# Performance work log

Measured on AMD Instinct MI355X. Metric: run time of the kernel, lower is better.

## Reference

```python
import jax, jax.numpy as jnp
import numpy as np

N_QUBITS = 4
N_LAYERS = 1
B, D_IN, D_OUT = 65536, 1024, 1024

def _cnot_perm(c, t):
    idx = np.arange(16)
    cb = (idx >> (3 - c)) & 1
    return idx ^ (cb << (3 - t))  # involutive permutation

CNOT_PERMS = [_cnot_perm(i, (i + 1) % N_QUBITS) for i in range(N_QUBITS)]
_idx = np.arange(16)
Z_SIGNS = np.stack([1.0 - 2.0 * ((_idx >> (3 - i)) & 1) for i in range(N_QUBITS)]).astype(np.float32)  # [4,16]
H_GATE = (np.array([[1, 1], [1, -1]]) / np.sqrt(2.0)).astype(np.complex64)

def _apply_1q(psi, U, wire):
    # psi: [B,2,2,2,2]; U: [2,2] (shared across batch)
    psi = jnp.moveaxis(psi, wire + 1, -1)
    psi = jnp.einsum('b...j,ij->b...i', psi, U)
    return jnp.moveaxis(psi, -1, wire + 1)

def _apply_1q_batched(psi, U, wire):
    # U: [B,2,2] (per-sample gate)
    psi = jnp.moveaxis(psi, wire + 1, -1)
    psi = jnp.einsum('b...j,bij->b...i', psi, U)
    return jnp.moveaxis(psi, -1, wire + 1)

def _ry_batched(th):
    c = jnp.cos(th / 2).astype(jnp.complex64)
    s = jnp.sin(th / 2).astype(jnp.complex64)
    return jnp.stack([jnp.stack([c, -s], -1), jnp.stack([s, c], -1)], -2)  # [B,2,2]

def _rz_batched(th):
    e = jnp.exp(-0.5j * th)  # complex64
    z = jnp.zeros_like(e)
    return jnp.stack([jnp.stack([e, z], -1), jnp.stack([z, jnp.conj(e)], -1)], -2)

def _rot(phi, th, om):
    # PennyLane Rot(phi,theta,omega) = RZ(omega) RY(theta) RZ(phi)
    c = jnp.cos(th / 2)
    s = jnp.sin(th / 2)
    return jnp.stack([
        jnp.stack([jnp.exp(-0.5j * (phi + om)) * c, -jnp.exp(0.5j * (phi - om)) * s]),
        jnp.stack([jnp.exp(-0.5j * (phi - om)) * s, jnp.exp(0.5j * (phi + om)) * c])])

def _circuit(angles, weights):
    # angles: [B,4] float; weights: [n_layers,4,3]; returns <Z_i> per wire: [B,4]
    b = angles.shape[0]
    psi = jnp.zeros((b, 16), jnp.complex64).at[:, 0].set(1.0).reshape(b, 2, 2, 2, 2)
    H = jnp.asarray(H_GATE)
    for i in range(N_QUBITS):
        psi = _apply_1q(psi, H, i)
        f = angles[:, i]
        psi = _apply_1q_batched(psi, _ry_batched(jnp.arctan(f)), i)
        psi = _apply_1q_batched(psi, _rz_batched(jnp.arctan(f ** 2)), i)
    for l in range(N_LAYERS):
        for i in range(N_QUBITS):
            psi = psi.reshape(b, 16)[:, CNOT_PERMS[i]].reshape(b, 2, 2, 2, 2)
        for i in range(N_QUBITS):
            U = _rot(weights[l, i, 0], weights[l, i, 1], weights[l, i, 2])
            psi = _apply_1q(psi, U, i)
    psi_f = psi.reshape(b, 16)
    probs = psi_f.real ** 2 + psi_f.imag ** 2  # [B,16] float32
    return probs @ jnp.asarray(Z_SIGNS).T  # [B,4]

def setup_inputs() -> dict:
    key = jax.random.key(0)
    k = jax.random.split(key, 6)
    scale_pre = 1.0 / np.sqrt(D_IN)
    scale_post = 1.0 / np.sqrt(N_QUBITS)
    return {
        'x': jax.random.normal(k[0], (B, D_IN), jnp.float32),
        'pre_w': jax.random.normal(k[1], (N_QUBITS, D_IN), jnp.float32) * scale_pre,
        'pre_b': jax.random.normal(k[2], (N_QUBITS,), jnp.float32) * scale_pre,
        'q_weights': jax.random.uniform(k[3], (N_LAYERS, N_QUBITS, 3), jnp.float32) * (2.0 * np.pi),
        'post_w': jax.random.normal(k[4], (D_OUT, N_QUBITS), jnp.float32) * scale_post,
        'post_b': jax.random.normal(k[5], (D_OUT,), jnp.float32) * scale_post,
    }

def reference(x, pre_w, pre_b, q_weights, post_w, post_b):
    h = jnp.tanh(x @ pre_w.T + pre_b) * np.pi  # [B,4]
    z = _circuit(h, q_weights).astype(jnp.float32)  # [B,4]
    return z @ post_w.T + post_b  # [B,1024]
```

## Files before the change

kernel.cpp:

```cpp
#include <hip/hip_runtime.h>
#include <math.h>

#define D_IN_K  1024
#define D_OUT_K 1024

static constexpr float PI_F = 3.14159265358979323846f;

__device__ __forceinline__ float dot4(float4 a, float4 b, float acc) {
    return fmaf(a.x, b.x, fmaf(a.y, b.y, fmaf(a.z, b.z, fmaf(a.w, b.w, acc))));
}

template <int MASK>
__device__ __forceinline__ void apply1q(
    float* pr, float* pim,
    float u00r, float u00i, float u01r, float u01i,
    float u10r, float u10i, float u11r, float u11i)
{
#pragma unroll
    for (int j = 0; j < 16; ++j) {
        if (j & MASK) continue;
        const int k = j | MASK;
        float a0r = pr[j], a0i = pim[j], a1r = pr[k], a1i = pim[k];
        pr[j]  = u00r * a0r - u00i * a0i + u01r * a1r - u01i * a1i;
        pim[j] = u00r * a0i + u00i * a0r + u01r * a1i + u01i * a1r;
        pr[k]  = u10r * a0r - u10i * a0i + u11r * a1r - u11i * a1i;
        pim[k] = u10r * a0i + u10i * a0r + u11r * a1i + u11i * a1r;
    }
}

template <int CMASK, int TMASK>
__device__ __forceinline__ void cnot(float* pr, float* pim)
{
#pragma unroll
    for (int j = 0; j < 16; ++j) {
        if ((j & CMASK) && !(j & TMASK)) {
            const int k = j | TMASK;
            float t;
            t = pr[j];  pr[j]  = pr[k];  pr[k]  = t;
            t = pim[j]; pim[j] = pim[k]; pim[k] = t;
        }
    }
}

template <int MASK>
__device__ __forceinline__ void encode_qubit(float* pr, float* pim, float f)
{
    const float r = 0.70710678118654752440f;
    apply1q<MASK>(pr, pim, r, 0.f, r, 0.f, r, 0.f, -r, 0.f);
    float th = atanf(f) * 0.5f;
    float s, c;
    sincosf(th, &s, &c);
    apply1q<MASK>(pr, pim, c, 0.f, -s, 0.f, s, 0.f, c, 0.f);
    float al = atanf(f * f) * 0.5f;
    float sa, ca;
    sincosf(al, &sa, &ca);
    apply1q<MASK>(pr, pim, ca, -sa, 0.f, 0.f, 0.f, 0.f, ca, sa);
}

template <int MASK>
__device__ __forceinline__ void rot_qubit(float* pr, float* pim,
                                          float phi, float th, float om)
{
    float st, ct, sp, cp, sm, cm;
    sincosf(0.5f * th, &st, &ct);
    sincosf(0.5f * (phi + om), &sp, &cp);
    sincosf(0.5f * (phi - om), &sm, &cm);
    apply1q<MASK>(pr, pim,
                  ct * cp, -ct * sp,
                  -st * cm, -st * sm,
                  st * cm, -st * sm,
                  ct * cp, ct * sp);
}

__global__ __launch_bounds__(256) void fused_kernel(
    const float* __restrict__ x, const float* __restrict__ pw,
    const float* __restrict__ pb, const float* __restrict__ qw,
    const float* __restrict__ postw, const float* __restrict__ postb,
    float* __restrict__ out, int B)
{
    const int t    = threadIdx.x;
    const int wave = t >> 6;
    const int lane = t & 63;
    const int row0  = blockIdx.x * 16;
    const int wrow0 = row0 + wave * 4;
    if (row0 >= B) return;

    __shared__ float4 zlds[16];

    const float4* pwv4 = reinterpret_cast<const float4*>(postw);
    float4 w[4];
    float bias[4];
#pragma unroll
    for (int j = 0; j < 4; ++j) {
        w[j]    = pwv4[t + 256 * j];
        bias[j] = postb[t + 256 * j];
    }

    const float4* w0 = reinterpret_cast<const float4*>(pw);
    const float4* w1 = reinterpret_cast<const float4*>(pw + D_IN_K);
    const float4* w2 = reinterpret_cast<const float4*>(pw + 2 * D_IN_K);
    const float4* w3 = reinterpret_cast<const float4*>(pw + 3 * D_IN_K);
    const float4* x0 = reinterpret_cast<const float4*>(x + (size_t)(wrow0 + 0) * D_IN_K);
    const float4* x1 = reinterpret_cast<const float4*>(x + (size_t)(wrow0 + 1) * D_IN_K);
    const float4* x2 = reinterpret_cast<const float4*>(x + (size_t)(wrow0 + 2) * D_IN_K);
    const float4* x3 = reinterpret_cast<const float4*>(x + (size_t)(wrow0 + 3) * D_IN_K);

    float acc[4][4];
#pragma unroll
    for (int r = 0; r < 4; ++r)
#pragma unroll
        for (int q = 0; q < 4; ++q) acc[r][q] = 0.f;

#pragma unroll
    for (int k = 0; k < 4; ++k) {
        const int idx = lane + (k << 6);
        float4 a = w0[idx], b = w1[idx], c = w2[idx], d = w3[idx];
        float4 xv;
        xv = x0[idx];
        acc[0][0] = dot4(xv, a, acc[0][0]); acc[0][1] = dot4(xv, b, acc[0][1]);
        acc[0][2] = dot4(xv, c, acc[0][2]); acc[0][3] = dot4(xv, d, acc[0][3]);
        xv = x1[idx];
        acc[1][0] = dot4(xv, a, acc[1][0]); acc[1][1] = dot4(xv, b, acc[1][1]);
        acc[1][2] = dot4(xv, c, acc[1][2]); acc[1][3] = dot4(xv, d, acc[1][3]);
        xv = x2[idx];
        acc[2][0] = dot4(xv, a, acc[2][0]); acc[2][1] = dot4(xv, b, acc[2][1]);
        acc[2][2] = dot4(xv, c, acc[2][2]); acc[2][3] = dot4(xv, d, acc[2][3]);
        xv = x3[idx];
        acc[3][0] = dot4(xv, a, acc[3][0]); acc[3][1] = dot4(xv, b, acc[3][1]);
        acc[3][2] = dot4(xv, c, acc[3][2]); acc[3][3] = dot4(xv, d, acc[3][3]);
    }

#pragma unroll
    for (int off = 1; off < 64; off <<= 1) {
#pragma unroll
        for (int r = 0; r < 4; ++r)
#pragma unroll
            for (int q = 0; q < 4; ++q)
                acc[r][q] += __shfl_xor(acc[r][q], off, 64);
    }

    if (lane < 4) {
        const int r = lane;
        float hq[4];
#pragma unroll
        for (int q = 0; q < 4; ++q)
            hq[q] = tanhf(acc[r][q] + pb[q]) * PI_F;

        float pr[16], pim[16];
#pragma unroll
        for (int j = 0; j < 16; ++j) { pr[j] = 0.f; pim[j] = 0.f; }
        pr[0] = 1.f;

        encode_qubit<8>(pr, pim, hq[0]);
        encode_qubit<4>(pr, pim, hq[1]);
        encode_qubit<2>(pr, pim, hq[2]);
        encode_qubit<1>(pr, pim, hq[3]);

        cnot<8, 4>(pr, pim);
        cnot<4, 2>(pr, pim);
        cnot<2, 1>(pr, pim);
        cnot<1, 8>(pr, pim);

        rot_qubit<8>(pr, pim, qw[0], qw[1], qw[2]);
        rot_qubit<4>(pr, pim, qw[3], qw[4], qw[5]);
        rot_qubit<2>(pr, pim, qw[6], qw[7], qw[8]);
        rot_qubit<1>(pr, pim, qw[9], qw[10], qw[11]);

        float z0 = 0.f, z1 = 0.f, z2 = 0.f, z3 = 0.f;
#pragma unroll
        for (int j = 0; j < 16; ++j) {
            float p = pr[j] * pr[j] + pim[j] * pim[j];
            z0 += (j & 8) ? -p : p;
            z1 += (j & 4) ? -p : p;
            z2 += (j & 2) ? -p : p;
            z3 += (j & 1) ? -p : p;
        }
        float4 zv; zv.x = z0; zv.y = z1; zv.z = z2; zv.w = z3;
        zlds[wave * 4 + r] = zv;
    }
    __syncthreads();

#pragma unroll
    for (int r = 0; r < 16; ++r) {
        float4 zr = zlds[r];
        float* orow = out + (size_t)(row0 + r) * D_OUT_K;
#pragma unroll
        for (int j = 0; j < 4; ++j) {
            float o = fmaf(zr.x, w[j].x,
                      fmaf(zr.y, w[j].y,
                      fmaf(zr.z, w[j].z,
                      fmaf(zr.w, w[j].w, bias[j]))));
            orow[t + 256 * j] = o;
        }
    }
}

extern "C" void kernel_launch(void* const* d_in, const int* in_sizes, int n_in,
                              void* d_out, int out_size, void* d_ws, size_t ws_size,
                              hipStream_t stream)
{
    const float* x      = (const float*)d_in[0];
    const float* pre_w  = (const float*)d_in[1];
    const float* pre_b  = (const float*)d_in[2];
    const float* qw     = (const float*)d_in[3];
    const float* post_w = (const float*)d_in[4];
    const float* post_b = (const float*)d_in[5];
    float* out = (float*)d_out;

    const int B = in_sizes[0] / D_IN_K;

    (void)d_ws; (void)ws_size;

    fused_kernel<<<(B + 15) / 16, 256, 0, stream>>>(
        x, pre_w, pre_b, qw, post_w, post_b, out, B);
}
```

Baseline: 445.5 us.

## Distribute quantum statevector across lanes and replace trig with algebraic identities

The 16-amplitude statevector simulation is now spread so each lane holds one amplitude, with one 16-lane group per batch row. It no longer runs serially in 4 lanes while 60 idle. The encoding stage is computed as a product state using cos/sin of half-arctan derived via sqrt identities instead of atanf/sincosf. CNOTs become lane shuffles, and the Z expectation uses a 16-lane butterfly. The output store is also changed to write one float4 per thread, with post weights loaded contiguously. Fast intrinsics (__sincosf) and the algebraic half-angle forms add small numerical differences.

New measurement: 461.6 us. +3.6%, slower.

```diff
diff --git a/kernel.cpp b/kernel.cpp
--- a/kernel.cpp
+++ b/kernel.cpp
@@ -4,72 +4,11 @@
 #define D_IN_K  1024
 #define D_OUT_K 1024
 
-static constexpr float PI_F = 3.14159265358979323846f;
+static constexpr float PI_F    = 3.14159265358979323846f;
+static constexpr float RSQRT2  = 0.70710678118654752440f;
 
 __device__ __forceinline__ float dot4(float4 a, float4 b, float acc) {
     return fmaf(a.x, b.x, fmaf(a.y, b.y, fmaf(a.z, b.z, fmaf(a.w, b.w, acc))));
-}
-
-template <int MASK>
-__device__ __forceinline__ void apply1q(
-    float* pr, float* pim,
-    float u00r, float u00i, float u01r, float u01i,
-    float u10r, float u10i, float u11r, float u11i)
-{
-#pragma unroll
-    for (int j = 0; j < 16; ++j) {
-        if (j & MASK) continue;
-        const int k = j | MASK;
-        float a0r = pr[j], a0i = pim[j], a1r = pr[k], a1i = pim[k];
-        pr[j]  = u00r * a0r - u00i * a0i + u01r * a1r - u01i * a1i;
-        pim[j] = u00r * a0i + u00i * a0r + u01r * a1i + u01i * a1r;
-        pr[k]  = u10r * a0r - u10i * a0i + u11r * a1r - u11i * a1i;
-        pim[k] = u10r * a0i + u10i * a0r + u11r * a1i + u11i * a1r;
-    }
-}
-
-template <int CMASK, int TMASK>
-__device__ __forceinline__ void cnot(float* pr, float* pim)
-{
-#pragma unroll
-    for (int j = 0; j < 16; ++j) {
-        if ((j & CMASK) && !(j & TMASK)) {
-            const int k = j | TMASK;
-            float t;
-            t = pr[j];  pr[j]  = pr[k];  pr[k]  = t;
-            t = pim[j]; pim[j] = pim[k]; pim[k] = t;
-        }
-    }
-}
-
-template <int MASK>
-__device__ __forceinline__ void encode_qubit(float* pr, float* pim, float f)
-{
-    const float r = 0.70710678118654752440f;
-    apply1q<MASK>(pr, pim, r, 0.f, r, 0.f, r, 0.f, -r, 0.f);
-    float th = atanf(f) * 0.5f;
-    float s, c;
-    sincosf(th, &s, &c);
-    apply1q<MASK>(pr, pim, c, 0.f, -s, 0.f, s, 0.f, c, 0.f);
-    float al = atanf(f * f) * 0.5f;
-    float sa, ca;
-    sincosf(al, &sa, &ca);
-    apply1q<MASK>(pr, pim, ca, -sa, 0.f, 0.f, 0.f, 0.f, ca, sa);
-}
-
-template <int MASK>
-__device__ __forceinline__ void rot_qubit(float* pr, float* pim,
-                                          float phi, float th, float om)
-{
-    float st, ct, sp, cp, sm, cm;
-    sincosf(0.5f * th, &st, &ct);
-    sincosf(0.5f * (phi + om), &sp, &cp);
-    sincosf(0.5f * (phi - om), &sm, &cm);
-    apply1q<MASK>(pr, pim,
-                  ct * cp, -ct * sp,
-                  -st * cm, -st * sm,
-                  st * cm, -st * sm,
-                  ct * cp, ct * sp);
 }
 
 __global__ __launch_bounds__(256) void fused_kernel(
@@ -81,6 +20,8 @@
     const int t    = threadIdx.x;
     const int wave = t >> 6;
     const int lane = t & 63;
+    const int amp  = lane & 15;
+    const int g    = lane >> 4;
     const int row0  = blockIdx.x * 16;
     const int wrow0 = row0 + wave * 4;
     if (row0 >= B) return;
@@ -89,12 +30,9 @@
 
     const float4* pwv4 = reinterpret_cast<const float4*>(postw);
     float4 w[4];
-    float bias[4];
-#pragma unroll
-    for (int j = 0; j < 4; ++j) {
-        w[j]    = pwv4[t + 256 * j];
-        bias[j] = postb[t + 256 * j];
-    }
+#pragma unroll
+    for (int j = 0; j < 4; ++j) w[j] = pwv4[4 * t + j];
+    float4 bias = reinterpret_cast<const float4*>(postb)[t];
 
     const float4* w0 = reinterpret_cast<const float4*>(pw);
     const float4* w1 = reinterpret_cast<const float4*>(pw + D_IN_K);
@@ -131,67 +69,120 @@
     }
 
 #pragma unroll
-    for (int off = 1; off < 64; off <<= 1) {
-#pragma unroll
-        for (int r = 0; r < 4; ++r)
-#pragma unroll
-            for (int q = 0; q < 4; ++q)
-                acc[r][q] += __shfl_xor(acc[r][q], off, 64);
-    }
-
-    if (lane < 4) {
-        const int r = lane;
-        float hq[4];
+    for (int r = 0; r < 4; ++r)
+#pragma unroll
+        for (int q = 0; q < 4; ++q) {
+            acc[r][q] += __shfl_xor(acc[r][q], 16, 64);
+            acc[r][q] += __shfl_xor(acc[r][q], 32, 64);
+        }
+
+    float myacc[4];
+#pragma unroll
+    for (int q = 0; q < 4; ++q) {
+        float v01 = (g & 1) ? acc[1][q] : acc[0][q];
+        float v23 = (g & 1) ? acc[3][q] : acc[2][q];
+        myacc[q] = (g & 2) ? v23 : v01;
+    }
+
+#pragma unroll
+    for (int off = 1; off < 16; off <<= 1)
 #pragma unroll
         for (int q = 0; q < 4; ++q)
-            hq[q] = tanhf(acc[r][q] + pb[q]) * PI_F;
-
-        float pr[16], pim[16];
-#pragma unroll
-        for (int j = 0; j < 16; ++j) { pr[j] = 0.f; pim[j] = 0.f; }
-        pr[0] = 1.f;
-
-        encode_qubit<8>(pr, pim, hq[0]);
-        encode_qubit<4>(pr, pim, hq[1]);
-        encode_qubit<2>(pr, pim, hq[2]);
-        encode_qubit<1>(pr, pim, hq[3]);
-
-        cnot<8, 4>(pr, pim);
-        cnot<4, 2>(pr, pim);
-        cnot<2, 1>(pr, pim);
-        cnot<1, 8>(pr, pim);
-
-        rot_qubit<8>(pr, pim, qw[0], qw[1], qw[2]);
-        rot_qubit<4>(pr, pim, qw[3], qw[4], qw[5]);
-        rot_qubit<2>(pr, pim, qw[6], qw[7], qw[8]);
-        rot_qubit<1>(pr, pim, qw[9], qw[10], qw[11]);
-
-        float z0 = 0.f, z1 = 0.f, z2 = 0.f, z3 = 0.f;
-#pragma unroll
-        for (int j = 0; j < 16; ++j) {
-            float p = pr[j] * pr[j] + pim[j] * pim[j];
-            z0 += (j & 8) ? -p : p;
-            z1 += (j & 4) ? -p : p;
-            z2 += (j & 2) ? -p : p;
-            z3 += (j & 1) ? -p : p;
+            myacc[q] += __shfl_xor(myacc[q], off, 64);
+
+    float hq[4];
+#pragma unroll
+    for (int q = 0; q < 4; ++q)
+        hq[q] = tanhf(myacc[q] + pb[q]) * PI_F;
+
+    float v0r[4], v0i[4], v1r[4], v1i[4];
+#pragma unroll
+    for (int q = 0; q < 4; ++q) {
+        float f   = hq[q];
+        float f2  = f * f;
+        float cth = 1.0f / sqrtf(fmaf(f,  f,  1.f));
+        float c   = sqrtf(0.5f * (1.f + cth));
+        float s   = copysignf(sqrtf(fmaxf(0.5f * (1.f - cth), 0.f)), f);
+        float cal = 1.0f / sqrtf(fmaf(f2, f2, 1.f));
+        float ca  = sqrtf(0.5f * (1.f + cal));
+        float sa  = sqrtf(fmaxf(0.5f * (1.f - cal), 0.f));
+        float a0  = RSQRT2 * (c - s);
+        float a1  = RSQRT2 * (c + s);
+        v0r[q] =  a0 * ca;  v0i[q] = -a0 * sa;
+        v1r[q] =  a1 * ca;  v1i[q] =  a1 * sa;
+    }
+
+    float ar, ai;
+    {
+        float x0r = (amp & 8) ? v1r[0] : v0r[0], x0i = (amp & 8) ? v1i[0] : v0i[0];
+        float x1r = (amp & 4) ? v1r[1] : v0r[1], x1i = (amp & 4) ? v1i[1] : v0i[1];
+        float x2r = (amp & 2) ? v1r[2] : v0r[2], x2i = (amp & 2) ? v1i[2] : v0i[2];
+        float x3r = (amp & 1) ? v1r[3] : v0r[3], x3i = (amp & 1) ? v1i[3] : v0i[3];
+        float m01r = x0r * x1r - x0i * x1i;
+        float m01i = x0r * x1i + x0i * x1r;
+        float m23r = x2r * x3r - x2i * x3i;
+        float m23i = x2r * x3i + x2i * x3r;
+        ar = m01r * m23r - m01i * m23i;
+        ai = m01r * m23i + m01i * m23r;
+    }
+
+    {
+        int src;
+        src = lane ^ ((lane & 8) ? 4 : 0);  ar = __shfl(ar, src, 64); ai = __shfl(ai, src, 64);
+        src = lane ^ ((lane & 4) ? 2 : 0);  ar = __shfl(ar, src, 64); ai = __shfl(ai, src, 64);
+        src = lane ^ ((lane & 2) ? 1 : 0);  ar = __shfl(ar, src, 64); ai = __shfl(ai, src, 64);
+        src = lane ^ ((lane & 1) ? 8 : 0);  ar = __shfl(ar, src, 64); ai = __shfl(ai, src, 64);
+    }
+
+#pragma unroll
+    for (int q = 0; q < 4; ++q) {
+        const int MASK = 8 >> q;
+        float phi = qw[3 * q + 0], th = qw[3 * q + 1], om = qw[3 * q + 2];
+        float st, ct, sp, cp, sm, cm;
+        __sincosf(0.5f * th, &st, &ct);
+        __sincosf(0.5f * (phi + om), &sp, &cp);
+        __sincosf(0.5f * (phi - om), &sm, &cm);
+        float br_ = __shfl_xor(ar, MASK, 64);
+        float bi_ = __shfl_xor(ai, MASK, 64);
+        bool  b   = (amp & MASK) != 0;
+        float cr = ct * cp;
+        float ci = b ? (ct * sp) : -(ct * sp);
+        float dr = b ? (st * cm) : -(st * cm);
+        float di = -st * sm;
+        float nar = cr * ar - ci * ai + dr * br_ - di * bi_;
+        float nai = cr * ai + ci * ar + dr * bi_ + di * br_;
+        ar = nar; ai = nai;
+    }
+
+    {
+        float p  = ar * ar + ai * ai;
+        float z0 = (amp & 8) ? -p : p;
+        float z1 = (amp & 4) ? -p : p;
+        float z2 = (amp & 2) ? -p : p;
+        float z3 = (amp & 1) ? -p : p;
+#pragma unroll
+        for (int off = 1; off < 16; off <<= 1) {
+            z0 += __shfl_xor(z0, off, 64);
+            z1 += __shfl_xor(z1, off, 64);
+            z2 += __shfl_xor(z2, off, 64);
+            z3 += __shfl_xor(z3, off, 64);
         }
-        float4 zv; zv.x = z0; zv.y = z1; zv.z = z2; zv.w = z3;
-        zlds[wave * 4 + r] = zv;
+        if (amp == 0) {
+            float4 zv; zv.x = z0; zv.y = z1; zv.z = z2; zv.w = z3;
+            zlds[wave * 4 + g] = zv;
+        }
     }
     __syncthreads();
 
 #pragma unroll
     for (int r = 0; r < 16; ++r) {
         float4 zr = zlds[r];
-        float* orow = out + (size_t)(row0 + r) * D_OUT_K;
-#pragma unroll
-        for (int j = 0; j < 4; ++j) {
-            float o = fmaf(zr.x, w[j].x,
-                      fmaf(zr.y, w[j].y,
-                      fmaf(zr.z, w[j].z,
-                      fmaf(zr.w, w[j].w, bias[j]))));
-            orow[t + 256 * j] = o;
-        }
+        float4 o;
+        o.x = fmaf(zr.x, w[0].x, fmaf(zr.y, w[0].y, fmaf(zr.z, w[0].z, fmaf(zr.w, w[0].w, bias.x))));
+        o.y = fmaf(zr.x, w[1].x, fmaf(zr.y, w[1].y, fmaf(zr.z, w[1].z, fmaf(zr.w, w[1].w, bias.y))));
+        o.z = fmaf(zr.x, w[2].x, fmaf(zr.y, w[2].y, fmaf(zr.z, w[2].z, fmaf(zr.w, w[2].w, bias.z))));
+        o.w = fmaf(zr.x, w[3].x, fmaf(zr.y, w[3].y, fmaf(zr.z, w[3].z, fmaf(zr.w, w[3].w, bias.w))));
+        reinterpret_cast<float4*>(out + (size_t)(row0 + r) * D_OUT_K)[t] = o;
     }
 }
 
```
